# Performance work log

Hardware: AMD Instinct MI355X
Metric: run time of the kernel (lower is better)

The kernel has to match this reference:

```python
import jax, jax.numpy as jnp
import numpy as np

N, D_IN, D_KQ, D_V = 4096, 1024, 1024, 1024


def setup_inputs() -> dict:
    key = jax.random.key(0)
    kx, kq, kk, kv = jax.random.split(key, 4)
    return {
        "x": jax.random.normal(kx, (N, D_IN), dtype=jnp.float32),
        "W_query": jax.random.uniform(kq, (D_IN, D_KQ), dtype=jnp.float32),
        "W_key": jax.random.uniform(kk, (D_IN, D_KQ), dtype=jnp.float32),
        "W_value": jax.random.uniform(kv, (D_IN, D_V), dtype=jnp.float32),
        "masked": 1,
    }


def reference(x, W_query, W_key, W_value, masked):
    # x: [N, d_in]; single-head, unbatched attention
    queries = x @ W_query          # [N, d_kq]
    keys = x @ W_key               # [N, d_kq]
    values = x @ W_value           # [N, d_v]
    scores = queries @ keys.T      # [N, N]
    if masked:  # masked is a static Python int
        n = x.shape[0]
        causal = jnp.triu(jnp.ones((n, n), dtype=bool), k=1)
        scores = jnp.where(causal, -jnp.inf, scores)
    scale = 1.0 / jnp.sqrt(jnp.asarray(W_key.shape[1], dtype=scores.dtype))
    attn = jax.nn.softmax(scores * scale, axis=-1)
    return attn @ values           # [N, d_v]
```

## Files before the change

kernel.cpp:

```cpp
#include <hip/hip_runtime.h>
#include <hip/hip_bf16.h>


using bf16 = __hip_bfloat16;
using f32x4 = __attribute__((ext_vector_type(4))) float;
using i32x4 = __attribute__((ext_vector_type(4))) int;
using i8 = signed char;

__device__ __forceinline__ void gload_lds16(const void* g, void* l) {
  __builtin_amdgcn_global_load_lds(
      (const __attribute__((address_space(1))) void*)g,
      (__attribute__((address_space(3))) void*)l, 16, 0, 0);
}

template <int ROWS, int CPR, int NT>
__device__ __forceinline__ void stage_tile8(const i8* __restrict__ g, i8* s,
                                            int ld) {
  const int t = threadIdx.x;
#pragma unroll
  for (int c = 0; c < ROWS * CPR / NT; ++c) {
    const int idx = c * NT + t;
    const int row = idx / CPR;
    const int ch = idx & (CPR - 1);
    const int cg = ch ^ ((row >> 1) & (CPR - 1));
    gload_lds16(g + (size_t)row * ld + cg * 16, s + idx * 16);
  }
}
template <int CPR>
__device__ __forceinline__ i32x4 frag_at8(const i8* s, int row, int ch) {
  return *(const i32x4*)&s[(row * CPR + (ch ^ ((row >> 1) & (CPR - 1)))) * 16];
}

__device__ __forceinline__ i32x4 mfma_i8(i32x4 a, i32x4 b, i32x4 c) {
  return __builtin_amdgcn_mfma_i32_16x16x64_i8(a, b, c, 0, 0, 0);
}

__global__ __launch_bounds__(256, 3) void gemm_qkv_i8(
    const i8* __restrict__ xh, const i8* __restrict__ xl,
    const i8* __restrict__ qTh, const i8* __restrict__ qTl,
    const i8* __restrict__ kTh, const i8* __restrict__ kTl,
    const i8* __restrict__ vTh, const i8* __restrict__ vTl,
    const float* __restrict__ srow, i8* __restrict__ Qh, i8* __restrict__ Ql,
    i8* __restrict__ Kh, i8* __restrict__ Kl, i8* __restrict__ VT) {
  __shared__ __align__(16) i8 sAh[128 * 64], sAl[128 * 64];
  __shared__ __align__(16) i8 sBh[64 * 64], sBl[64 * 64];

  const int bx = blockIdx.x;
  const int which = bx >> 4;
  const int n0 = (bx & 15) * 64;
  const int m0 = blockIdx.y * 128;
  const i8* Bh = which == 0 ? qTh : which == 1 ? kTh : vTh;
  const i8* Bl = which == 0 ? qTl : which == 1 ? kTl : vTl;
  const i8* A_h = xh + (size_t)m0 * 1024;
  const i8* A_l = xl + (size_t)m0 * 1024;
  const i8* B_h = Bh + (size_t)n0 * 1024;
  const i8* B_l = Bl + (size_t)n0 * 1024;

  const int t = threadIdx.x, lane = t & 63, w = t >> 6;
  const int wr = (w >> 1) * 64, wc = (w & 1) * 32;
  const int frow = lane & 15, fc = lane >> 4;

  i32x4 a0[4][2], a1[4][2];
#pragma unroll
  for (int i = 0; i < 4; ++i)
#pragma unroll
    for (int j = 0; j < 2; ++j) {
      a0[i][j] = (i32x4){0, 0, 0, 0};
      a1[i][j] = (i32x4){0, 0, 0, 0};
    }

  for (int kt = 0; kt < 16; ++kt) {
    const int k0 = kt * 64;
    stage_tile8<128, 4, 256>(A_h + k0, sAh, 1024);
    stage_tile8<64, 4, 256>(B_h + k0, sBh, 1024);
    stage_tile8<128, 4, 256>(A_l + k0, sAl, 1024);
    stage_tile8<64, 4, 256>(B_l + k0, sBl, 1024);
    __syncthreads();

    i32x4 ah[4], al[4], bh[2], bl[2];
#pragma unroll
    for (int i = 0; i < 4; ++i) {
      ah[i] = frag_at8<4>(sAh, wr + i * 16 + frow, fc);
      al[i] = frag_at8<4>(sAl, wr + i * 16 + frow, fc);
    }
#pragma unroll
    for (int j = 0; j < 2; ++j) {
      bh[j] = frag_at8<4>(sBh, wc + j * 16 + frow, fc);
      bl[j] = frag_at8<4>(sBl, wc + j * 16 + frow, fc);
    }
#pragma unroll
    for (int i = 0; i < 4; ++i)
#pragma unroll
      for (int j = 0; j < 2; ++j) {
        a0[i][j] = mfma_i8(ah[i], bh[j], a0[i][j]);
        a1[i][j] = mfma_i8(ah[i], bl[j], a1[i][j]);
        a1[i][j] = mfma_i8(al[i], bh[j], a1[i][j]);
      }
    __syncthreads();
  }

  const int er = (lane >> 4) * 4, ec = lane & 15;
  if (which < 2) {
    i8* Ph = which == 0 ? Qh : Kh;
    i8* Pl = which == 0 ? Ql : Kl;
#pragma unroll
    for (int i = 0; i < 4; ++i)
#pragma unroll
      for (int j = 0; j < 2; ++j)
#pragma unroll
        for (int r = 0; r < 4; ++r) {
          const int gm = m0 + wr + i * 16 + er + r;
          const int gn = n0 + wc + j * 16 + ec;
          const float Qf =
              65536.f * (float)a0[i][j][r] + 256.f * (float)a1[i][j][r];
          int q16 = __float2int_rn(Qf * (1.f / 262144.f));
          q16 = min(max(q16, -32511), 32511);
          const int h = (q16 + 128) >> 8;
          const int l = q16 - (h << 8);
          const size_t off = (size_t)gm * 1024 + gn;
          Ph[off] = (i8)h;
          Pl[off] = (i8)l;
        }
  } else {
    const int gm_base = m0 + wr;
#pragma unroll
    for (int i = 0; i < 4; ++i)
#pragma unroll
      for (int j = 0; j < 2; ++j) {
        const int gn = n0 + wc + j * 16 + ec;
        uint pk = 0;
#pragma unroll
        for (int r = 0; r < 4; ++r) {
          const int gm = gm_base + i * 16 + er + r;
          const float Vf =
              (65536.f * (float)a0[i][j][r] + 256.f * (float)a1[i][j][r]) *
                  (1.f / 134217728.f) +
              0.5f * srow[gm];
          int v8 = __float2int_rn(Vf);
          v8 = min(max(v8, -127), 127);
          pk |= (uint)(v8 & 255) << (8 * r);
        }
        *(uint*)(VT + (size_t)gn * 4096 + gm_base + i * 16 + er) = pk;
      }
  }
}

__global__ __launch_bounds__(256, 3) void gemm_s_i8(
    const i8* __restrict__ Qh, const i8* __restrict__ Ql,
    const i8* __restrict__ Kh, const i8* __restrict__ Kl,
    const float* __restrict__ srow, const float* __restrict__ qsum,
    const float* __restrict__ ksum, float* __restrict__ S) {
  const int cb = blockIdx.x, rb = blockIdx.y;
  if (cb > 2 * rb + 1) return;
  const int n0 = cb * 64, m0 = rb * 128;
  __shared__ __align__(16) i8 sAh[128 * 64], sAl[128 * 64];
  __shared__ __align__(16) i8 sBh[64 * 64], sBl[64 * 64];

  const i8* A_h = Qh + (size_t)m0 * 1024;
  const i8* A_l = Ql + (size_t)m0 * 1024;
  const i8* B_h = Kh + (size_t)n0 * 1024;
  const i8* B_l = Kl + (size_t)n0 * 1024;

  const int t = threadIdx.x, lane = t & 63, w = t >> 6;
  const int wr = (w >> 1) * 64, wc = (w & 1) * 32;
  const int frow = lane & 15, fc = lane >> 4;

  i32x4 a0[4][2], a1[4][2];
#pragma unroll
  for (int i = 0; i < 4; ++i)
#pragma unroll
    for (int j = 0; j < 2; ++j) {
      a0[i][j] = (i32x4){0, 0, 0, 0};
      a1[i][j] = (i32x4){0, 0, 0, 0};
    }

  for (int kt = 0; kt < 16; ++kt) {
    const int k0 = kt * 64;
    stage_tile8<128, 4, 256>(A_h + k0, sAh, 1024);
    stage_tile8<64, 4, 256>(B_h + k0, sBh, 1024);
    stage_tile8<128, 4, 256>(A_l + k0, sAl, 1024);
    stage_tile8<64, 4, 256>(B_l + k0, sBl, 1024);
    __syncthreads();

    i32x4 ah[4], al[4], bh[2], bl[2];
#pragma unroll
    for (int i = 0; i < 4; ++i) {
      ah[i] = frag_at8<4>(sAh, wr + i * 16 + frow, fc);
      al[i] = frag_at8<4>(sAl, wr + i * 16 + frow, fc);
    }
#pragma unroll
    for (int j = 0; j < 2; ++j) {
      bh[j] = frag_at8<4>(sBh, wc + j * 16 + frow, fc);
      bl[j] = frag_at8<4>(sBl, wc + j * 16 + frow, fc);
    }
#pragma unroll
    for (int i = 0; i < 4; ++i)
#pragma unroll
      for (int j = 0; j < 2; ++j) {
        a0[i][j] = mfma_i8(ah[i], bh[j], a0[i][j]);
        a1[i][j] = mfma_i8(ah[i], bl[j], a1[i][j]);
        a1[i][j] = mfma_i8(al[i], bh[j], a1[i][j]);
      }
    __syncthreads();
  }

  const int er = (lane >> 4) * 4, ec = lane & 15;
  float sn[2], kn[2];
#pragma unroll
  for (int j = 0; j < 2; ++j) {
    const int gn = n0 + wc + j * 16 + ec;
    sn[j] = srow[gn];
    kn[j] = ksum[gn];
  }
#pragma unroll
  for (int i = 0; i < 4; ++i)
#pragma unroll
    for (int r = 0; r < 4; ++r) {
      const int gm = m0 + wr + i * 16 + er + r;
      const float sm = srow[gm], qm = qsum[gm];
#pragma unroll
      for (int j = 0; j < 2; ++j) {
        const int gn = n0 + wc + j * 16 + ec;
        const float Sf =
            65536.f * (float)a0[i][j][r] + 256.f * (float)a1[i][j][r];
        const float logit = Sf * (1.f / 8388608.f) +
                            0.015625f * (sn[j] * qm + sm * kn[j]) +
                            8.f * sm * sn[j];
        S[(size_t)gm * 4096 + gn] = logit;
      }
    }
}

__global__ __launch_bounds__(256, 4) void gemm_pv_i8(
    const i8* __restrict__ P, const i8* __restrict__ VT,
    const float* __restrict__ inv_s, float* __restrict__ O) {
  __shared__ __align__(16) i8 sP[128 * 64];
  __shared__ __align__(16) i8 sV[64 * 64];

  const int cid = blockIdx.x;
  const int h = cid >> 8;
  const int idx = cid & 255;
  const int rb = h ? (31 - (idx >> 3)) : (idx >> 3);
  const int m0 = rb * 128;
  const int n0 = ((idx & 7) + 8 * h) * 64;
  const int ktiles = 2 * (rb + 1);

  const i8* A0 = P + (size_t)m0 * 4096;
  const i8* B0 = VT + (size_t)n0 * 4096;

  const int t = threadIdx.x, lane = t & 63, w = t >> 6;
  const int wr = (w >> 1) * 64, wc = (w & 1) * 32;
  const int frow = lane & 15, fc = lane >> 4;

  i32x4 a0[4][2];
#pragma unroll
  for (int i = 0; i < 4; ++i)
#pragma unroll
    for (int j = 0; j < 2; ++j) a0[i][j] = (i32x4){0, 0, 0, 0};

  for (int kt = 0; kt < ktiles; ++kt) {
    const int k0 = kt * 64;
    stage_tile8<128, 4, 256>(A0 + k0, sP, 4096);
    stage_tile8<64, 4, 256>(B0 + k0, sV, 4096);
    __syncthreads();

    i32x4 pa[4], b[2];
#pragma unroll
    for (int i = 0; i < 4; ++i) pa[i] = frag_at8<4>(sP, wr + i * 16 + frow, fc);
#pragma unroll
    for (int j = 0; j < 2; ++j) b[j] = frag_at8<4>(sV, wc + j * 16 + frow, fc);
#pragma unroll
    for (int i = 0; i < 4; ++i)
#pragma unroll
      for (int j = 0; j < 2; ++j) a0[i][j] = mfma_i8(pa[i], b[j], a0[i][j]);
    __syncthreads();
  }

  const int er = (lane >> 4) * 4, ec = lane & 15;
#pragma unroll
  for (int i = 0; i < 4; ++i)
#pragma unroll
    for (int j = 0; j < 2; ++j)
#pragma unroll
      for (int r = 0; r < 4; ++r) {
        const int gm = m0 + wr + i * 16 + er + r;
        const int gn = n0 + wc + j * 16 + ec;
        O[(size_t)gm * 1024 + gn] =
            (float)a0[i][j][r] * inv_s[gm] * (1.f / 127.f);
      }
}

__global__ __launch_bounds__(256) void softmax_kernel(
    const float* __restrict__ S, i8* __restrict__ P,
    float* __restrict__ inv_s, int N) {
  const int wid = threadIdx.x >> 6;
  const int r0 = blockIdx.x * 2 + (wid >> 1);
  const int row = (wid & 1) ? (N - 1 - r0) : r0;
  const int lane = threadIdx.x & 63;
  const float* s = S + (size_t)row * N;
  i8* p = P + (size_t)row * N;
  const int len = row + 1;
  const int nv4 = len >> 2;
  const float4* s4 = (const float4*)s;

  float m = -3.4e38f;
  for (int j = lane; j < nv4; j += 64) {
    const float4 v = s4[j];
    m = fmaxf(m, fmaxf(fmaxf(v.x, v.y), fmaxf(v.z, v.w)));
  }
  for (int j = (nv4 << 2) + lane; j < len; j += 64) m = fmaxf(m, s[j]);
#pragma unroll
  for (int off = 32; off > 0; off >>= 1) m = fmaxf(m, __shfl_xor(m, off, 64));

  float sum = 0.f;
  for (int j = lane; j < nv4; j += 64) {
    const float4 v = s4[j];
    const float e0 = __expf(v.x - m), e1 = __expf(v.y - m);
    const float e2 = __expf(v.z - m), e3 = __expf(v.w - m);
    sum += (e0 + e1) + (e2 + e3);
    uint pk = (uint)__float2int_rn(e0 * 127.f);
    pk |= (uint)__float2int_rn(e1 * 127.f) << 8;
    pk |= (uint)__float2int_rn(e2 * 127.f) << 16;
    pk |= (uint)__float2int_rn(e3 * 127.f) << 24;
    *(uint*)(p + 4 * j) = pk;
  }
  for (int j = (nv4 << 2) + lane; j < len; j += 64) {
    const float e = __expf(s[j] - m);
    sum += e;
    p[j] = (i8)__float2int_rn(e * 127.f);
  }
#pragma unroll
  for (int off = 32; off > 0; off >>= 1) sum += __shfl_xor(sum, off, 64);

  const int bound = ((row >> 7) + 1) << 7;
  for (int j = len + lane; j < bound; j += 64) p[j] = (i8)0;
  if (lane == 0) inv_s[row] = 1.f / sum;
}

__global__ __launch_bounds__(256) void fused_x_rowstats(
    const float* __restrict__ x, const float* __restrict__ wqrow,
    const float* __restrict__ wkrow, uint* __restrict__ xh,
    uint* __restrict__ xl, float* __restrict__ srow, float* __restrict__ qsum,
    float* __restrict__ ksum) {
  const int row = blockIdx.x * 4 + (threadIdx.x >> 6);
  const int lane = threadIdx.x & 63;
  const float4* r4 = (const float4*)(x + (size_t)row * 1024);
  const float4* wq4 = (const float4*)wqrow;
  const float4* wk4 = (const float4*)wkrow;
  uint* h4 = xh + (size_t)row * 256;
  uint* l4 = xl + (size_t)row * 256;

  float ss = 0.f, sq = 0.f, sk = 0.f;
  for (int j = lane; j < 256; j += 64) {
    const float4 v = r4[j];
    const float4 wq = wq4[j];
    const float4 wk = wk4[j];
    const float f[4] = {v.x, v.y, v.z, v.w};
    ss += (v.x + v.y) + (v.z + v.w);
    sq += v.x * wq.x + v.y * wq.y + v.z * wq.z + v.w * wq.w;
    sk += v.x * wk.x + v.y * wk.y + v.z * wk.z + v.w * wk.w;
    uint hp = 0, lp = 0;
#pragma unroll
    for (int k = 0; k < 4; ++k) {
      int q = __float2int_rn(f[k] * 4096.f);
      q = min(max(q, -32511), 32511);
      const int hh = (q + 128) >> 8;
      const int ll = q - (hh << 8);
      hp |= (uint)(hh & 255) << (8 * k);
      lp |= (uint)(ll & 255) << (8 * k);
    }
    h4[j] = hp;
    l4[j] = lp;
  }
#pragma unroll
  for (int off = 32; off > 0; off >>= 1) {
    ss += __shfl_xor(ss, off, 64);
    sq += __shfl_xor(sq, off, 64);
    sk += __shfl_xor(sk, off, 64);
  }
  if (lane == 0) {
    srow[row] = ss;
    qsum[row] = sq;
    ksum[row] = sk;
  }
}

__global__ void split_transpose_w_i8(
    const float* __restrict__ W0, const float* __restrict__ W1,
    const float* __restrict__ W2, i8* __restrict__ T0h, i8* __restrict__ T0l,
    i8* __restrict__ T1h, i8* __restrict__ T1l, i8* __restrict__ T2h,
    i8* __restrict__ T2l, int R, int C) {
  const int z = blockIdx.z;
  const float* W = z == 0 ? W0 : z == 1 ? W1 : W2;
  i8* Th = z == 0 ? T0h : z == 1 ? T1h : T2h;
  i8* Tl = z == 0 ? T0l : z == 1 ? T1l : T2l;
  __shared__ float tile[32][33];
  const int c0 = blockIdx.x * 32, r0 = blockIdx.y * 32;
  const int tx = threadIdx.x, ty = threadIdx.y;
  for (int rr = ty; rr < 32; rr += 8)
    tile[rr][tx] = W[(size_t)(r0 + rr) * C + c0 + tx];
  __syncthreads();
  for (int cc = ty; cc < 32; cc += 8) {
    const float v = tile[tx][cc] - 0.5f;
    int w16 = __float2int_rn(v * 32768.f);
    w16 = min(max(w16, -32511), 32511);
    const int h = (w16 + 128) >> 8;
    const int l = w16 - (h << 8);
    const size_t off = (size_t)(c0 + cc) * R + r0 + tx;
    Th[off] = (i8)h;
    Tl[off] = (i8)l;
  }
}

__global__ __launch_bounds__(256) void wrow_kernel(const float* __restrict__ Wq,
                                                   const float* __restrict__ Wk,
                                                   float* __restrict__ wqrow,
                                                   float* __restrict__ wkrow) {
  const int k = blockIdx.x * 4 + (threadIdx.x >> 6);
  const int lane = threadIdx.x & 63;
  const float* W = blockIdx.y == 0 ? Wq : Wk;
  float* out = blockIdx.y == 0 ? wqrow : wkrow;
  const float* row = W + (size_t)k * 1024;
  float s = 0.f;
  for (int c = lane; c < 1024; c += 64) s += row[c];
#pragma unroll
  for (int off = 32; off > 0; off >>= 1) s += __shfl_xor(s, off, 64);
  if (lane == 0) out[k] = s - 512.f;
}

extern "C" void kernel_launch(void* const* d_in, const int* in_sizes, int n_in,
                              void* d_out, int out_size, void* d_ws,
                              size_t ws_size, hipStream_t stream) {
  (void)in_sizes; (void)n_in; (void)out_size; (void)ws_size;
  const float* x = (const float*)d_in[0];
  const float* Wq = (const float*)d_in[1];
  const float* Wk = (const float*)d_in[2];
  const float* Wv = (const float*)d_in[3];

  const int N = 4096, D = 1024;

  char* p = (char*)d_ws;
  auto alloc = [&](size_t bytes) {
    char* r = p;
    p += (bytes + 255) & ~(size_t)255;
    return r;
  };
  i8* xh = (i8*)alloc((size_t)N * D);
  i8* xl = (i8*)alloc((size_t)N * D);
  i8* WqTh = (i8*)alloc((size_t)D * D);
  i8* WqTl = (i8*)alloc((size_t)D * D);
  i8* WkTh = (i8*)alloc((size_t)D * D);
  i8* WkTl = (i8*)alloc((size_t)D * D);
  i8* WvTh = (i8*)alloc((size_t)D * D);
  i8* WvTl = (i8*)alloc((size_t)D * D);
  i8* Qh = (i8*)alloc((size_t)N * D);
  i8* Ql = (i8*)alloc((size_t)N * D);
  i8* Kh = (i8*)alloc((size_t)N * D);
  i8* Kl = (i8*)alloc((size_t)N * D);
  i8* VT = (i8*)alloc((size_t)D * N);
  float* S = (float*)alloc((size_t)N * N * 4);
  i8* P = (i8*)alloc((size_t)N * N);
  float* inv_s = (float*)alloc((size_t)N * 4);
  float* srow = (float*)alloc((size_t)N * 4);
  float* qsum = (float*)alloc((size_t)N * 4);
  float* ksum = (float*)alloc((size_t)N * 4);
  float* wqrow = (float*)alloc((size_t)D * 4);
  float* wkrow = (float*)alloc((size_t)D * 4);

  wrow_kernel<<<dim3(D / 4, 2), 256, 0, stream>>>(Wq, Wk, wqrow, wkrow);
  split_transpose_w_i8<<<dim3(32, 32, 3), dim3(32, 8), 0, stream>>>(
      Wq, Wk, Wv, WqTh, WqTl, WkTh, WkTl, WvTh, WvTl, D, D);
  fused_x_rowstats<<<N / 4, 256, 0, stream>>>(x, wqrow, wkrow, (uint*)xh,
                                              (uint*)xl, srow, qsum, ksum);

  gemm_qkv_i8<<<dim3(48, 32), 256, 0, stream>>>(xh, xl, WqTh, WqTl, WkTh, WkTl,
                                                WvTh, WvTl, srow, Qh, Ql, Kh,
                                                Kl, VT);

  gemm_s_i8<<<dim3(64, 32), 256, 0, stream>>>(Qh, Ql, Kh, Kl, srow, qsum, ksum,
                                              S);

  softmax_kernel<<<N / 4, 256, 0, stream>>>(S, P, inv_s, N);

  gemm_pv_i8<<<512, 256, 0, stream>>>(P, VT, inv_s, (float*)d_out);
}
```

Baseline: 235.3 us.

## Double-buffer LDS tiles with async prefetch in all int8 GEMM kernels

Converts the three int8 MFMA GEMM kernels (QKV projection, scores, PV) from single-buffered staging to double-buffered LDS. The next K-tile's global-to-LDS loads are issued before computing on the current one, with explicit vmcnt waits and raw barriers in place of __syncthreads. It also raises wave priority around the MFMA block. The aim is to hide global load latency behind matrix math, at the cost of doubled LDS per block, which may lower occupancy. The hand-counted vmcnt values must match the number of loads issued.

```diff
diff --git a/kernel.cpp b/kernel.cpp
--- a/kernel.cpp
+++ b/kernel.cpp
@@ -33,6 +33,20 @@
 
 __device__ __forceinline__ i32x4 mfma_i8(i32x4 a, i32x4 b, i32x4 c) {
   return __builtin_amdgcn_mfma_i32_16x16x64_i8(a, b, c, 0, 0, 0);
+}
+
+__device__ __forceinline__ void wait_vm6() {
+  asm volatile("s_waitcnt vmcnt(6)" ::: "memory");
+}
+__device__ __forceinline__ void wait_vm3() {
+  asm volatile("s_waitcnt vmcnt(3)" ::: "memory");
+}
+__device__ __forceinline__ void wait_vm0() {
+  asm volatile("s_waitcnt vmcnt(0)" ::: "memory");
+}
+__device__ __forceinline__ void barrier_pipe() {
+  __builtin_amdgcn_s_barrier();
+  __builtin_amdgcn_sched_barrier(0);
 }
 
 __global__ __launch_bounds__(256, 3) void gemm_qkv_i8(
@@ -42,8 +56,8 @@
     const i8* __restrict__ vTh, const i8* __restrict__ vTl,
     const float* __restrict__ srow, i8* __restrict__ Qh, i8* __restrict__ Ql,
     i8* __restrict__ Kh, i8* __restrict__ Kl, i8* __restrict__ VT) {
-  __shared__ __align__(16) i8 sAh[128 * 64], sAl[128 * 64];
-  __shared__ __align__(16) i8 sBh[64 * 64], sBl[64 * 64];
+  __shared__ __align__(16) i8 sAh[2][128 * 64], sAl[2][128 * 64];
+  __shared__ __align__(16) i8 sBh[2][64 * 64], sBl[2][64 * 64];
 
   const int bx = blockIdx.x;
   const int which = bx >> 4;
@@ -69,25 +83,38 @@
       a1[i][j] = (i32x4){0, 0, 0, 0};
     }
 
+  auto stage_all = [&](int kt, int b) {
+    const int k0 = kt * 64;
+    stage_tile8<128, 4, 256>(A_h + k0, sAh[b], 1024);
+    stage_tile8<64, 4, 256>(B_h + k0, sBh[b], 1024);
+    stage_tile8<128, 4, 256>(A_l + k0, sAl[b], 1024);
+    stage_tile8<64, 4, 256>(B_l + k0, sBl[b], 1024);
+  };
+
+  stage_all(0, 0);
   for (int kt = 0; kt < 16; ++kt) {
-    const int k0 = kt * 64;
-    stage_tile8<128, 4, 256>(A_h + k0, sAh, 1024);
-    stage_tile8<64, 4, 256>(B_h + k0, sBh, 1024);
-    stage_tile8<128, 4, 256>(A_l + k0, sAl, 1024);
-    stage_tile8<64, 4, 256>(B_l + k0, sBl, 1024);
-    __syncthreads();
+    const int cur = kt & 1;
+    if (kt < 15) {
+      stage_all(kt + 1, cur ^ 1);
+      wait_vm6();
+    } else {
+      wait_vm0();
+    }
+    barrier_pipe();
 
     i32x4 ah[4], al[4], bh[2], bl[2];
 #pragma unroll
     for (int i = 0; i < 4; ++i) {
-      ah[i] = frag_at8<4>(sAh, wr + i * 16 + frow, fc);
-      al[i] = frag_at8<4>(sAl, wr + i * 16 + frow, fc);
+      ah[i] = frag_at8<4>(sAh[cur], wr + i * 16 + frow, fc);
+      al[i] = frag_at8<4>(sAl[cur], wr + i * 16 + frow, fc);
     }
 #pragma unroll
     for (int j = 0; j < 2; ++j) {
-      bh[j] = frag_at8<4>(sBh, wc + j * 16 + frow, fc);
-      bl[j] = frag_at8<4>(sBl, wc + j * 16 + frow, fc);
-    }
+      bh[j] = frag_at8<4>(sBh[cur], wc + j * 16 + frow, fc);
+      bl[j] = frag_at8<4>(sBl[cur], wc + j * 16 + frow, fc);
+    }
+
+    __builtin_amdgcn_s_setprio(1);
 #pragma unroll
     for (int i = 0; i < 4; ++i)
 #pragma unroll
@@ -96,7 +123,8 @@
         a1[i][j] = mfma_i8(ah[i], bl[j], a1[i][j]);
         a1[i][j] = mfma_i8(al[i], bh[j], a1[i][j]);
       }
-    __syncthreads();
+    __builtin_amdgcn_s_setprio(0);
+    barrier_pipe();
   }
 
   const int er = (lane >> 4) * 4, ec = lane & 15;
@@ -153,8 +181,8 @@
   const int cb = blockIdx.x, rb = blockIdx.y;
   if (cb > 2 * rb + 1) return;
   const int n0 = cb * 64, m0 = rb * 128;
-  __shared__ __align__(16) i8 sAh[128 * 64], sAl[128 * 64];
-  __shared__ __align__(16) i8 sBh[64 * 64], sBl[64 * 64];
+  __shared__ __align__(16) i8 sAh[2][128 * 64], sAl[2][128 * 64];
+  __shared__ __align__(16) i8 sBh[2][64 * 64], sBl[2][64 * 64];
 
   const i8* A_h = Qh + (size_t)m0 * 1024;
   const i8* A_l = Ql + (size_t)m0 * 1024;
@@ -174,25 +202,38 @@
       a1[i][j] = (i32x4){0, 0, 0, 0};
     }
 
+  auto stage_all = [&](int kt, int b) {
+    const int k0 = kt * 64;
+    stage_tile8<128, 4, 256>(A_h + k0, sAh[b], 1024);
+    stage_tile8<64, 4, 256>(B_h + k0, sBh[b], 1024);
+    stage_tile8<128, 4, 256>(A_l + k0, sAl[b], 1024);
+    stage_tile8<64, 4, 256>(B_l + k0, sBl[b], 1024);
+  };
+
+  stage_all(0, 0);
   for (int kt = 0; kt < 16; ++kt) {
-    const int k0 = kt * 64;
-    stage_tile8<128, 4, 256>(A_h + k0, sAh, 1024);
-    stage_tile8<64, 4, 256>(B_h + k0, sBh, 1024);
-    stage_tile8<128, 4, 256>(A_l + k0, sAl, 1024);
-    stage_tile8<64, 4, 256>(B_l + k0, sBl, 1024);
-    __syncthreads();
+    const int cur = kt & 1;
+    if (kt < 15) {
+      stage_all(kt + 1, cur ^ 1);
+      wait_vm6();
+    } else {
+      wait_vm0();
+    }
+    barrier_pipe();
 
     i32x4 ah[4], al[4], bh[2], bl[2];
 #pragma unroll
     for (int i = 0; i < 4; ++i) {
-      ah[i] = frag_at8<4>(sAh, wr + i * 16 + frow, fc);
-      al[i] = frag_at8<4>(sAl, wr + i * 16 + frow, fc);
+      ah[i] = frag_at8<4>(sAh[cur], wr + i * 16 + frow, fc);
+      al[i] = frag_at8<4>(sAl[cur], wr + i * 16 + frow, fc);
     }
 #pragma unroll
     for (int j = 0; j < 2; ++j) {
-      bh[j] = frag_at8<4>(sBh, wc + j * 16 + frow, fc);
-      bl[j] = frag_at8<4>(sBl, wc + j * 16 + frow, fc);
-    }
+      bh[j] = frag_at8<4>(sBh[cur], wc + j * 16 + frow, fc);
+      bl[j] = frag_at8<4>(sBl[cur], wc + j * 16 + frow, fc);
+    }
+
+    __builtin_amdgcn_s_setprio(1);
 #pragma unroll
     for (int i = 0; i < 4; ++i)
 #pragma unroll
@@ -201,7 +242,8 @@
         a1[i][j] = mfma_i8(ah[i], bl[j], a1[i][j]);
         a1[i][j] = mfma_i8(al[i], bh[j], a1[i][j]);
       }
-    __syncthreads();
+    __builtin_amdgcn_s_setprio(0);
+    barrier_pipe();
   }
 
   const int er = (lane >> 4) * 4, ec = lane & 15;
@@ -234,8 +276,8 @@
 __global__ __launch_bounds__(256, 4) void gemm_pv_i8(
     const i8* __restrict__ P, const i8* __restrict__ VT,
     const float* __restrict__ inv_s, float* __restrict__ O) {
-  __shared__ __align__(16) i8 sP[128 * 64];
-  __shared__ __align__(16) i8 sV[64 * 64];
+  __shared__ __align__(16) i8 sP[2][128 * 64];
+  __shared__ __align__(16) i8 sV[2][64 * 64];
 
   const int cid = blockIdx.x;
   const int h = cid >> 8;
@@ -258,22 +300,38 @@
 #pragma unroll
     for (int j = 0; j < 2; ++j) a0[i][j] = (i32x4){0, 0, 0, 0};
 
+  auto stage_all = [&](int kt, int b) {
+    const int k0 = kt * 64;
+    stage_tile8<128, 4, 256>(A0 + k0, sP[b], 4096);
+    stage_tile8<64, 4, 256>(B0 + k0, sV[b], 4096);
+  };
+
+  stage_all(0, 0);
   for (int kt = 0; kt < ktiles; ++kt) {
-    const int k0 = kt * 64;
-    stage_tile8<128, 4, 256>(A0 + k0, sP, 4096);
-    stage_tile8<64, 4, 256>(B0 + k0, sV, 4096);
-    __syncthreads();
+    const int cur = kt & 1;
+    if (kt + 1 < ktiles) {
+      stage_all(kt + 1, cur ^ 1);
+      wait_vm3();
+    } else {
+      wait_vm0();
+    }
+    barrier_pipe();
 
     i32x4 pa[4], b[2];
 #pragma unroll
-    for (int i = 0; i < 4; ++i) pa[i] = frag_at8<4>(sP, wr + i * 16 + frow, fc);
-#pragma unroll
-    for (int j = 0; j < 2; ++j) b[j] = frag_at8<4>(sV, wc + j * 16 + frow, fc);
-#pragma unroll
     for (int i = 0; i < 4; ++i)
+      pa[i] = frag_at8<4>(sP[cur], wr + i * 16 + frow, fc);
+#pragma unroll
+    for (int j = 0; j < 2; ++j)
+      b[j] = frag_at8<4>(sV[cur], wc + j * 16 + frow, fc);
+
+    __builtin_amdgcn_s_setprio(1);
+#pragma unroll
+    for (int i = 0; i < 4; ++i)
 #pragma unroll
       for (int j = 0; j < 2; ++j) a0[i][j] = mfma_i8(pa[i], b[j], a0[i][j]);
-    __syncthreads();
+    __builtin_amdgcn_s_setprio(0);
+    barrier_pipe();
   }
 
   const int er = (lane >> 4) * 4, ec = lane & 15;
```

Result: faster. 229.8 us (-2.3%).
